# Kernel optimization log

Hardware: AMD Instinct MI355X
Metric: run time of the kernel (lower is better)

The kernel has to match this reference:

```python
import jax, jax.numpy as jnp
import numpy as np
from jax import lax

B, NL, W = 1024, 64, 2048
EPS_N = 1e-8   # added to n in m12 denominator (as in torch source)
EPS_Y = 1e-9   # added to E before admittance division (as in torch source)


def setup_inputs() -> dict:
    key = jax.random.key(0)
    k1, k2 = jax.random.split(key)
    # refractive indices of typical dielectrics, thicknesses ~quarter-wave in nm
    n_layers = 1.0 + 1.5 * jax.random.uniform(k1, (B, NL), dtype=jnp.float32)
    d_layers = 20.0 + 200.0 * jax.random.uniform(k2, (B, NL), dtype=jnp.float32)
    wavelengths = jnp.linspace(400.0, 800.0, W, dtype=jnp.float32)
    return {"n_layers": n_layers, "d_layers": d_layers, "wavelengths": wavelengths}


def reference(n_layers, d_layers, wavelengths):
    # n_layers: (B, N) real -> complex64; d_layers: (B, N) nm; wavelengths: (W,) nm
    n = n_layers.astype(jnp.complex64)
    k0 = (2.0 * np.pi / wavelengths).astype(jnp.complex64)  # (W,)
    num_layers = n.shape[1]

    def step(M, nd):
        # M: (B, W, 2, 2) complex64 running product; nd = (n_i, d_i) each (B,)
        n_i, d_i = nd
        phi = n_i[:, None] * d_i[:, None] * k0[None, :]          # (B, W)
        c = jnp.cos(phi)
        s = jnp.sin(phi)
        m12 = -1j * s / (n_i[:, None] + EPS_N)
        m21 = -1j * n_i[:, None] * s
        # layer characteristic matrix (B, W, 2, 2)
        M_layer = jnp.stack(
            [jnp.stack([c, m12], axis=-1), jnp.stack([m21, c], axis=-1)],
            axis=-2,
        )
        M_new = jnp.einsum("bwij,bwjk->bwik", M, M_layer)
        return M_new, None

    M0 = jnp.broadcast_to(
        jnp.eye(2, dtype=jnp.complex64), (n.shape[0], k0.shape[0], 2, 2)
    )
    # scan over interior layers 1 .. N-2 (substrate/ambient are semi-infinite)
    xs = (n[:, 1 : num_layers - 1].T, d_layers[:, 1 : num_layers - 1].T)
    M, _ = lax.scan(step, M0, xs)

    n_in = n[:, 0]    # (B,) incident-side index
    n_sub = n[:, -1]  # (B,) substrate index
    # EH = M @ [1, n_sub]^T  ->  E, H : (B, W)
    E = M[..., 0, 0] + M[..., 0, 1] * n_sub[:, None]
    H = M[..., 1, 0] + M[..., 1, 1] * n_sub[:, None]
    Y = H / (E + EPS_Y)
    r = (n_in[:, None] - Y) / (n_in[:, None] + Y)
    R = jnp.abs(r) ** 2
    return R.astype(jnp.float32)
```

## Files before the change

### kernel.cpp

```cpp
#include <hip/hip_runtime.h>
#include <math.h>

constexpr int B  = 1024;
constexpr int NL = 64;
constexpr int W  = 2048;
constexpr int INNER = NL - 2;
constexpr float EPS_N = 1e-8f;
constexpr float EPS_Y = 1e-9f;

typedef float v2f __attribute__((ext_vector_type(2)));

__global__ __launch_bounds__(256)
void tmm_kernel(const float* __restrict__ n_layers,
                const float* __restrict__ d_layers,
                const float* __restrict__ wavelengths,
                float* __restrict__ out)
{
    __shared__ float4 s_layer[INNER];
    __shared__ float s_edge[2];

    const int b   = blockIdx.y;
    const int tid = threadIdx.x;
    const int w   = blockIdx.x * 256 + tid;

    if (tid < INNER) {
        const float n = n_layers[b * NL + 1 + tid];
        const float d = d_layers[b * NL + 1 + tid];
        s_layer[tid] = make_float4(n * d, n, -n, 1.0f / (n + EPS_N));
    }
    if (tid == INNER) {
        s_edge[0] = n_layers[b * NL];
        s_edge[1] = n_layers[b * NL + NL - 1];
    }
    __syncthreads();

    const float inv_lambda = 1.0f / wavelengths[w];

    v2f p = {1.0f, 0.0f};
    v2f q = {0.0f, 1.0f};

    #pragma unroll
    for (int i = 0; i < INNER; ++i) {
        const float4 L = s_layer[i];
        const float phi_rev = L.x * inv_lambda;
        const float s = __builtin_amdgcn_sinf(phi_rev);
        const float c = __builtin_amdgcn_cosf(phi_rev);

        const v2f nn  = {L.y, L.z};
        const v2f ss  = {s, s};
        const v2f ns2 = nn * ss;
        const float is = L.w * s;
        const v2f is2 = {-is, is};
        const v2f c2  = {c, c};

        const v2f pold = p;
        p = __builtin_elementwise_fma(q,    ns2, p * c2);
        q = __builtin_elementwise_fma(pold, is2, q * c2);
    }

    const float a  = p.x;
    const float cc = p.y;
    const float bb = q.x;
    const float dd = q.y;

    const float n_in  = s_edge[0];
    const float n_sub = s_edge[1];

    const float Er = a + EPS_Y;
    const float Ei = bb * n_sub;
    const float Hr = dd * n_sub;
    const float Hi = cc;

    const float Nr = fmaf(n_in, Er, -Hr);
    const float Ni = fmaf(n_in, Ei, -Hi);
    const float Dr = fmaf(n_in, Er,  Hr);
    const float Di = fmaf(n_in, Ei,  Hi);

    const float R = (Nr * Nr + Ni * Ni) / (Dr * Dr + Di * Di);
    out[b * W + w] = R;
}

extern "C" void kernel_launch(void* const* d_in, const int* in_sizes, int n_in,
                              void* d_out, int out_size, void* d_ws, size_t ws_size,
                              hipStream_t stream)
{
    const float* n_layers    = (const float*)d_in[0];
    const float* d_layers    = (const float*)d_in[1];
    const float* wavelengths = (const float*)d_in[2];
    float* out = (float*)d_out;

    dim3 grid(W / 256, B);
    dim3 block(256);
    tmm_kernel<<<grid, block, 0, stream>>>(n_layers, d_layers, wavelengths, out);
}
```

Before: 104.1 us.

## Replace hardware sin/cos with packed polynomial over layer pairs

Processes two layers per iteration and computes sin and cos with a packed-FP32 polynomial (half-angle sine and cosine, then double-angle identities) instead of the transcendental sin/cos instructions. All arithmetic is issued as inline v_pk_* assembly with op_sel broadcasts and neg modifiers. The aim is to move work off the quarter-rate transcendental unit onto full-rate packed FMA pipes. In exchange it adds many more VALU ops per layer, uses hand-written asm that limits compiler scheduling, and carries a polynomial accuracy risk.

```diff
diff --git a/kernel.cpp b/kernel.cpp
--- a/kernel.cpp
+++ b/kernel.cpp
@@ -5,10 +5,41 @@
 constexpr int NL = 64;
 constexpr int W  = 2048;
 constexpr int INNER = NL - 2;
+constexpr int NG = INNER / 2;
 constexpr float EPS_N = 1e-8f;
 constexpr float EPS_Y = 1e-9f;
 
 typedef float v2f __attribute__((ext_vector_type(2)));
+
+#define PK_MUL(d,a,b)   asm("v_pk_mul_f32 %0, %1, %2" : "=v"(d) : "v"(a), "v"(b))
+#define PK_ADD(d,a,b)   asm("v_pk_add_f32 %0, %1, %2" : "=v"(d) : "v"(a), "v"(b))
+#define PK_SUB(d,a,b)   asm("v_pk_add_f32 %0, %1, %2 neg_lo:[0,1] neg_hi:[0,1]" : "=v"(d) : "v"(a), "v"(b))
+#define PK_FMA(d,a,b,c) asm("v_pk_fma_f32 %0, %1, %2, %3" : "=v"(d) : "v"(a), "v"(b), "v"(c))
+#define PK_MUL_BCLO(d,a,b) \
+  asm("v_pk_mul_f32 %0, %1, %2 op_sel:[0,0] op_sel_hi:[1,0]" : "=v"(d) : "v"(a), "v"(b))
+#define PK_MUL_BCHI(d,a,b) \
+  asm("v_pk_mul_f32 %0, %1, %2 op_sel:[0,1] op_sel_hi:[1,1]" : "=v"(d) : "v"(a), "v"(b))
+#define PK_FMA_BCLO_NEGHI(d,a,b,c) \
+  asm("v_pk_fma_f32 %0, %1, %2, %3 op_sel:[0,0,0] op_sel_hi:[1,0,1] neg_hi:[0,1,0]" : "=v"(d) : "v"(a), "v"(b), "v"(c))
+#define PK_FMA_BCHI_NEGHI(d,a,b,c) \
+  asm("v_pk_fma_f32 %0, %1, %2, %3 op_sel:[0,1,0] op_sel_hi:[1,1,1] neg_hi:[0,1,0]" : "=v"(d) : "v"(a), "v"(b), "v"(c))
+#define PK_FMA_BCLO_NEGLO(d,a,b,c) \
+  asm("v_pk_fma_f32 %0, %1, %2, %3 op_sel:[0,0,0] op_sel_hi:[1,0,1] neg_lo:[0,1,0]" : "=v"(d) : "v"(a), "v"(b), "v"(c))
+#define PK_FMA_BCHI_NEGLO(d,a,b,c) \
+  asm("v_pk_fma_f32 %0, %1, %2, %3 op_sel:[0,1,0] op_sel_hi:[1,1,1] neg_lo:[0,1,0]" : "=v"(d) : "v"(a), "v"(b), "v"(c))
+
+#define A0 3.14159265358979f
+#define A1 -5.16771278004997f
+#define A2 2.55016403987735f
+#define A3 -0.599264529320792f
+#define A4 0.0821458866111282f
+#define A5 -0.00737043094571435f
+#define B0 1.0f
+#define B1 -4.93480220054468f
+#define B2 4.05871212641677f
+#define B3 -1.33526276885459f
+#define B4 0.235330630358514f
+#define B5 -0.0258068914490399f
 
 __global__ __launch_bounds__(256)
 void tmm_kernel(const float* __restrict__ n_layers,
@@ -16,46 +47,84 @@
                 const float* __restrict__ wavelengths,
                 float* __restrict__ out)
 {
-    __shared__ float4 s_layer[INNER];
+    __shared__ v2f s_nd[NG];
+    __shared__ v2f s_n[NG];
+    __shared__ v2f s_rn[NG];
     __shared__ float s_edge[2];
 
     const int b   = blockIdx.y;
     const int tid = threadIdx.x;
     const int w   = blockIdx.x * 256 + tid;
 
-    if (tid < INNER) {
-        const float n = n_layers[b * NL + 1 + tid];
-        const float d = d_layers[b * NL + 1 + tid];
-        s_layer[tid] = make_float4(n * d, n, -n, 1.0f / (n + EPS_N));
+    if (tid < NG) {
+        const int base = b * NL + 1 + 2 * tid;
+        const float n0 = n_layers[base],     n1 = n_layers[base + 1];
+        const float d0 = d_layers[base],     d1 = d_layers[base + 1];
+        v2f nd = {n0 * d0, n1 * d1};
+        v2f nn = {n0, n1};
+        v2f rn = {1.0f / (n0 + EPS_N), 1.0f / (n1 + EPS_N)};
+        s_nd[tid] = nd;
+        s_n[tid]  = nn;
+        s_rn[tid] = rn;
     }
-    if (tid == INNER) {
+    if (tid == NG) {
         s_edge[0] = n_layers[b * NL];
         s_edge[1] = n_layers[b * NL + NL - 1];
     }
     __syncthreads();
 
-    const float inv_lambda = 1.0f / wavelengths[w];
+    const float il = 1.0f / wavelengths[w];
+    const v2f il2 = {il, il};
+    const v2f A5P = {A5, A5}, A4P = {A4, A4}, A3P = {A3, A3},
+              A2P = {A2, A2}, A1P = {A1, A1}, A0P = {A0, A0};
+    const v2f B5P = {B5, B5}, B4P = {B4, B4}, B3P = {B3, B3},
+              B2P = {B2, B2}, B1P = {B1, B1}, B0P = {B0, B0};
+    const v2f ONEP = {1.0f, 1.0f};
 
     v2f p = {1.0f, 0.0f};
     v2f q = {0.0f, 1.0f};
 
     #pragma unroll
-    for (int i = 0; i < INNER; ++i) {
-        const float4 L = s_layer[i];
-        const float phi_rev = L.x * inv_lambda;
-        const float s = __builtin_amdgcn_sinf(phi_rev);
-        const float c = __builtin_amdgcn_cosf(phi_rev);
+    for (int g = 0; g < NG; ++g) {
+        const v2f nd2 = s_nd[g];
+        const v2f n2  = s_n[g];
+        const v2f rn2 = s_rn[g];
 
-        const v2f nn  = {L.y, L.z};
-        const v2f ss  = {s, s};
-        const v2f ns2 = nn * ss;
-        const float is = L.w * s;
-        const v2f is2 = {-is, is};
-        const v2f c2  = {c, c};
+        v2f phi; PK_MUL(phi, nd2, il2);
+        v2f rnd = {__builtin_rintf(phi.x), __builtin_rintf(phi.y)};
+        v2f r;   PK_SUB(r, phi, rnd);
+        v2f y2;  PK_MUL(y2, r, r);
 
-        const v2f pold = p;
-        p = __builtin_elementwise_fma(q,    ns2, p * c2);
-        q = __builtin_elementwise_fma(pold, is2, q * c2);
+        v2f sh;  PK_FMA(sh, y2, A5P, A4P);
+                 PK_FMA(sh, y2, sh, A3P);
+                 PK_FMA(sh, y2, sh, A2P);
+                 PK_FMA(sh, y2, sh, A1P);
+                 PK_FMA(sh, y2, sh, A0P);
+                 PK_MUL(sh, sh, r);
+        v2f ch;  PK_FMA(ch, y2, B5P, B4P);
+                 PK_FMA(ch, y2, ch, B3P);
+                 PK_FMA(ch, y2, ch, B2P);
+                 PK_FMA(ch, y2, ch, B1P);
+                 PK_FMA(ch, y2, ch, B0P);
+        v2f sh2; PK_ADD(sh2, sh, sh);
+        v2f s;   PK_MUL(s, sh2, ch);
+        v2f t2;  PK_MUL(t2, sh2, sh);
+        v2f c;   PK_SUB(c, ONEP, t2);
+
+        v2f nsp; PK_MUL(nsp, n2, s);
+        v2f isp; PK_MUL(isp, rn2, s);
+
+        v2f t0, pn, t1, qn;
+        PK_MUL_BCLO(t0, p, c);
+        PK_FMA_BCLO_NEGHI(pn, q, nsp, t0);
+        PK_MUL_BCLO(t1, q, c);
+        PK_FMA_BCLO_NEGLO(qn, p, isp, t1);
+        p = pn; q = qn;
+        PK_MUL_BCHI(t0, p, c);
+        PK_FMA_BCHI_NEGHI(pn, q, nsp, t0);
+        PK_MUL_BCHI(t1, q, c);
+        PK_FMA_BCHI_NEGLO(qn, p, isp, t1);
+        p = pn; q = qn;
     }
 
     const float a  = p.x;
```

Measured after the change: 121.1 us. +16.3%, slower.
